# Kernel tuning notes

Measured on AMD Instinct MI355X. Metric: run time of the kernel, lower is better.

Reference implementation:

```python
import jax, jax.numpy as jnp
import numpy as np

NB_X = 32
NB_Y = 32
EPS = 1e-08


def setup_inputs() -> dict:
    key = jax.random.key(0)
    ks = jax.random.split(key, 10)
    B, L, F, H, D = 16, NB_X * NB_Y + 1, 768, 12, 64
    s = 0.02
    return {
        'x': jax.random.normal(ks[0], (B, L, F), dtype=jnp.float32),
        'wq': jax.random.normal(ks[1], (F, H, D), dtype=jnp.float32) * s,
        'bq': jnp.zeros((H, D), dtype=jnp.float32),
        'wk': jax.random.normal(ks[2], (F, H, D), dtype=jnp.float32) * s,
        'bk': jnp.zeros((H, D), dtype=jnp.float32),
        'wv': jax.random.normal(ks[3], (F, H, D), dtype=jnp.float32) * s,
        'bv': jnp.zeros((H, D), dtype=jnp.float32),
        'wo': jax.random.normal(ks[4], (H, D, F), dtype=jnp.float32) * s,
        'bo': jnp.zeros((F,), dtype=jnp.float32),
        'toeplitz_params': jax.random.normal(ks[5], (H, 4 * NB_X * NB_Y), dtype=jnp.float32),
    }


def _dist_index():
    # relative-position index over the 2D patch grid, flattened to (L0*L0,)
    gi = np.arange(NB_X)
    gj = np.arange(NB_Y)
    idx = ((gi[:, None, None, None] - gi[None, None, :, None] + NB_X) * 2 * NB_Y
           + gj[None, :, None, None] - gj[None, None, None, :] + NB_Y)
    return jnp.asarray(idx.reshape(-1), dtype=jnp.int32)


def reference(x, wq, bq, wk, bk, wv, bv, wo, bo, toeplitz_params):
    H, D = wq.shape[1], wq.shape[2]
    L0 = NB_X * NB_Y  # number of patch tokens (seq len = L0 + 1 with CLS)

    q = jnp.einsum('bqf,fhd->bqhd', x, wq) + bq
    k = jnp.einsum('bkf,fhd->bkhd', x, wk) + bk
    v = jnp.einsum('bkf,fhd->bkhd', x, wv) + bv

    # relu-kernelized scores
    q = jax.nn.relu(q / jnp.sqrt(jnp.float32(D))) + EPS
    k = jax.nn.relu(k) + EPS
    attn = jnp.einsum('bqhd,bkhd->bhqk', q, k)  # [B,H,L,L]

    # per-head Toeplitz relative-position mask via gather
    tm = jnp.take(toeplitz_params, _dist_index(), axis=1).reshape(H, L0, L0)
    tm = jnp.pad(tm, [[0, 0], [1, 0], [0, 0]], constant_values=1.0)
    tm = jnp.pad(tm, [[0, 0], [0, 0], [1, 0]], constant_values=1.0)

    attn = attn * jnp.abs(tm)[None] + EPS
    attn = attn / jnp.sum(attn, axis=-1, keepdims=True)  # sum-normalization

    out = jnp.einsum('bhqk,bkhd->bqhd', attn, v)
    return jnp.einsum('bqhd,hdf->bqf', out, wo) + bo
```

## Files before the change

kernel.cpp:

```cpp
#include <hip/hip_runtime.h>
#include <hip/hip_bf16.h>

#define BB 16
#define LQ 1025
#define FF 768
#define HH 12
#define DD 64
#define EPSF 1e-8f

typedef unsigned short u16;
typedef __attribute__((ext_vector_type(8))) short  bf16x8;
typedef __attribute__((ext_vector_type(4))) float  f32x4;

__device__ __forceinline__ float bf2f(u16 u) {
    union { unsigned int i; float f; } c;
    c.i = ((unsigned int)u) << 16;
    return c.f;
}

__device__ __forceinline__ u16 f2bf(float f) {
    union { float f; unsigned int i; } c;
    c.f = f;
    unsigned int x = c.i;
    unsigned int r = (x + 0x7fffu + ((x >> 16) & 1u)) >> 16;
    return (u16)r;
}

__global__ __launch_bounds__(256) void convert_x(
    const float* __restrict__ x, u16* __restrict__ xb, int n4)
{
    int i = blockIdx.x * blockDim.x + threadIdx.x;
    const int stride = gridDim.x * blockDim.x;
    for (; i < n4; i += stride) {
        float4 f = ((const float4*)x)[i];
        ushort4 o;
        o.x = f2bf(f.x); o.y = f2bf(f.y); o.z = f2bf(f.z); o.w = f2bf(f.w);
        ((ushort4*)xb)[i] = o;
    }
}

__global__ __launch_bounds__(256) void transpose_w(
    const float* __restrict__ wq, const float* __restrict__ wk,
    const float* __restrict__ wv, const float* __restrict__ wo,
    u16* __restrict__ wqt, u16* __restrict__ wkt,
    u16* __restrict__ wvt, u16* __restrict__ wot)
{
    const int z = blockIdx.z;
    const float* __restrict__ src = (z == 0) ? wq : (z == 1) ? wk : (z == 2) ? wv : wo;
    u16* __restrict__ dst         = (z == 0) ? wqt : (z == 1) ? wkt : (z == 2) ? wvt : wot;

    const int c0 = blockIdx.x * 64;
    const int r0 = blockIdx.y * 64;

    __shared__ u16 tile[64][72];

    const int t   = threadIdx.x;
    const int row = t >> 2;
    const int cs  = (t & 3) << 4;

    {
        const float* p = src + (size_t)(r0 + row) * 768 + c0 + cs;
#pragma unroll
        for (int q = 0; q < 4; ++q) {
            float4 f = *(const float4*)(p + 4 * q);
            ushort4 o;
            o.x = f2bf(f.x); o.y = f2bf(f.y); o.z = f2bf(f.z); o.w = f2bf(f.w);
            *(ushort4*)&tile[row][cs + 4 * q] = o;
        }
    }
    __syncthreads();
    {
        u16* p = dst + (size_t)(c0 + row) * 768 + r0 + cs;
#pragma unroll
        for (int q = 0; q < 4; ++q) {
            ushort4 o;
            o.x = tile[cs + 4 * q + 0][row];
            o.y = tile[cs + 4 * q + 1][row];
            o.z = tile[cs + 4 * q + 2][row];
            o.w = tile[cs + 4 * q + 3][row];
            *(ushort4*)(p + 4 * q) = o;
        }
    }
}

__global__ __launch_bounds__(256) void gemm_qkv_mfma(
    const u16* __restrict__ xb,
    const u16* __restrict__ wqt, const u16* __restrict__ wkt,
    const u16* __restrict__ wvt,
    const float* __restrict__ bq, const float* __restrict__ bk,
    const float* __restrict__ bv,
    u16* __restrict__ qbuf, u16* __restrict__ kbuf, u16* __restrict__ vbuf)
{
    const int M  = BB * LQ;
    const int m0 = blockIdx.x * 128;
    const int h  = blockIdx.y;
    const int n0 = h * 64;

    __shared__ u16 As[128][40];
    __shared__ u16 Bq[64][40];
    __shared__ u16 Bk[64][40];
    __shared__ u16 Bv[64][40];

    const int t    = threadIdx.x;
    const int wave = t >> 6;
    const int lane = t & 63;
    const int quad = lane >> 4;
    const int l16  = lane & 15;

    const int sm   = t >> 1;
    const int sseg = (t & 1) << 4;
    const int bn   = t >> 2;
    const int bseg = (t & 3) << 3;

    f32x4 acc[3][2][4];
#pragma unroll
    for (int ty = 0; ty < 3; ++ty)
#pragma unroll
        for (int i = 0; i < 2; ++i)
#pragma unroll
            for (int j = 0; j < 4; ++j)
                acc[ty][i][j] = (f32x4){0.f, 0.f, 0.f, 0.f};

    for (int k0 = 0; k0 < 768; k0 += 32) {
        __syncthreads();
        {
            int gm = m0 + sm;
            if (gm < M) {
                const uint4* p = (const uint4*)(xb + (size_t)gm * 768 + k0 + sseg);
                *(uint4*)&As[sm][sseg]     = p[0];
                *(uint4*)&As[sm][sseg + 8] = p[1];
            } else {
                uint4 z; z.x = 0; z.y = 0; z.z = 0; z.w = 0;
                *(uint4*)&As[sm][sseg]     = z;
                *(uint4*)&As[sm][sseg + 8] = z;
            }
        }
        {
            size_t off = (size_t)(n0 + bn) * 768 + k0 + bseg;
            *(uint4*)&Bq[bn][bseg] = *(const uint4*)(wqt + off);
            *(uint4*)&Bk[bn][bseg] = *(const uint4*)(wkt + off);
            *(uint4*)&Bv[bn][bseg] = *(const uint4*)(wvt + off);
        }
        __syncthreads();

        bf16x8 af0 = *(const bf16x8*)&As[(wave << 5) + l16][quad * 8];
        bf16x8 af1 = *(const bf16x8*)&As[(wave << 5) + 16 + l16][quad * 8];
#pragma unroll
        for (int j = 0; j < 4; ++j) {
            bf16x8 bq8 = *(const bf16x8*)&Bq[16 * j + l16][quad * 8];
            acc[0][0][j] = __builtin_amdgcn_mfma_f32_16x16x32_bf16(af0, bq8, acc[0][0][j], 0, 0, 0);
            acc[0][1][j] = __builtin_amdgcn_mfma_f32_16x16x32_bf16(af1, bq8, acc[0][1][j], 0, 0, 0);
            bf16x8 bk8 = *(const bf16x8*)&Bk[16 * j + l16][quad * 8];
            acc[1][0][j] = __builtin_amdgcn_mfma_f32_16x16x32_bf16(af0, bk8, acc[1][0][j], 0, 0, 0);
            acc[1][1][j] = __builtin_amdgcn_mfma_f32_16x16x32_bf16(af1, bk8, acc[1][1][j], 0, 0, 0);
            bf16x8 bv8 = *(const bf16x8*)&Bv[16 * j + l16][quad * 8];
            acc[2][0][j] = __builtin_amdgcn_mfma_f32_16x16x32_bf16(af0, bv8, acc[2][0][j], 0, 0, 0);
            acc[2][1][j] = __builtin_amdgcn_mfma_f32_16x16x32_bf16(af1, bv8, acc[2][1][j], 0, 0, 0);
        }
    }

#pragma unroll
    for (int i = 0; i < 2; ++i) {
#pragma unroll
        for (int reg = 0; reg < 4; ++reg) {
            int gm = m0 + (wave << 5) + (i << 4) + quad * 4 + reg;
            if (gm >= M) continue;
            int b_idx = gm / LQ;
            int l     = gm - b_idx * LQ;
            size_t obase = ((size_t)(b_idx * HH + h) * LQ + l) * 64;
#pragma unroll
            for (int j = 0; j < 4; ++j) {
                int d = 16 * j + l16;
                float fb = bq[n0 + d];
                float vq = acc[0][i][j][reg] + fb;
                vq = fmaxf(vq * 0.125f, 0.f) + EPSF;
                qbuf[obase + d] = f2bf(vq);
                float vk = acc[1][i][j][reg] + bk[n0 + d];
                vk = fmaxf(vk, 0.f) + EPSF;
                kbuf[obase + d] = f2bf(vk);
                float vv = acc[2][i][j][reg] + bv[n0 + d];
                vbuf[obase + d] = f2bf(vv);
            }
        }
    }
}

__global__ __launch_bounds__(256) void attn_fused(
    const u16* __restrict__ qbuf, const u16* __restrict__ kbuf,
    const u16* __restrict__ vbuf, const float* __restrict__ tp,
    u16* __restrict__ obuf)
{
    const int bh = blockIdx.y;
    const int b  = bh / HH;
    const int h  = bh - b * HH;
    const int q0 = blockIdx.x * 64;

    __shared__ u16 SQ[64][72];
    __shared__ u16 Ks[64][72];
    __shared__ u16 Vt[64][72];

    const int t    = threadIdx.x;
    const int wave = t >> 6;
    const int lane = t & 63;
    const int quad = lane >> 4;
    const int l16  = lane & 15;
    const int w16  = wave << 4;

    const size_t base  = (size_t)bh * LQ * 64;
    const int    hbase = h * 4096;

    {
        const int row = t >> 2;
        const int s0  = (t & 3) << 4;
        const int qi = q0 + row;
        if (qi < LQ) {
            const uint4* qp = (const uint4*)(qbuf + base + (size_t)qi * 64 + s0);
            *(uint4*)&SQ[row][s0]     = qp[0];
            *(uint4*)&SQ[row][s0 + 8] = qp[1];
        } else {
            uint4 z; z.x = 0; z.y = 0; z.z = 0; z.w = 0;
            *(uint4*)&SQ[row][s0]     = z;
            *(uint4*)&SQ[row][s0 + 8] = z;
        }
    }
    __syncthreads();

    bf16x8 qf0 = *(const bf16x8*)&SQ[w16 + l16][quad * 8];
    bf16x8 qf1 = *(const bf16x8*)&SQ[w16 + l16][32 + quad * 8];

    int  gqi_[4], gqj_[4];
    bool qv_[4], qc_[4];
#pragma unroll
    for (int reg = 0; reg < 4; ++reg) {
        int qi = q0 + w16 + quad * 4 + reg;
        qv_[reg] = (qi < LQ);
        qc_[reg] = (qi == 0);
        int qm1 = qi - 1;
        gqi_[reg] = (qv_[reg] && !qc_[reg]) ? (qm1 >> 5) : 0;
        gqj_[reg] = (qv_[reg] && !qc_[reg]) ? (qm1 & 31) : 0;
    }

    f32x4 acc_o[4];
#pragma unroll
    for (int dt = 0; dt < 4; ++dt) acc_o[dt] = (f32x4){0.f, 0.f, 0.f, 0.f};
    float den_acc[4] = {0.f, 0.f, 0.f, 0.f};

    for (int kt = 0; kt < 17; ++kt) {
        const int k0 = kt * 64;
        __syncthreads();

        {
            const int row = t >> 2;
            const int s0  = (t & 3) << 4;
            const int ki = k0 + row;
            if (ki < LQ) {
                const uint4* kp = (const uint4*)(kbuf + base + (size_t)ki * 64 + s0);
                *(uint4*)&Ks[row][s0]     = kp[0];
                *(uint4*)&Ks[row][s0 + 8] = kp[1];
                const ushort4* vp = (const ushort4*)(vbuf + base + (size_t)ki * 64 + s0);
                ushort4 v0 = vp[0], v1 = vp[1], v2 = vp[2], v3 = vp[3];
                Vt[s0 +  0][row] = v0.x; Vt[s0 +  1][row] = v0.y;
                Vt[s0 +  2][row] = v0.z; Vt[s0 +  3][row] = v0.w;
                Vt[s0 +  4][row] = v1.x; Vt[s0 +  5][row] = v1.y;
                Vt[s0 +  6][row] = v1.z; Vt[s0 +  7][row] = v1.w;
                Vt[s0 +  8][row] = v2.x; Vt[s0 +  9][row] = v2.y;
                Vt[s0 + 10][row] = v2.z; Vt[s0 + 11][row] = v2.w;
                Vt[s0 + 12][row] = v3.x; Vt[s0 + 13][row] = v3.y;
                Vt[s0 + 14][row] = v3.z; Vt[s0 + 15][row] = v3.w;
            } else {
                uint4 z; z.x = 0; z.y = 0; z.z = 0; z.w = 0;
                *(uint4*)&Ks[row][s0]     = z;
                *(uint4*)&Ks[row][s0 + 8] = z;
#pragma unroll
                for (int j = 0; j < 16; ++j) Vt[s0 + j][row] = 0;
            }
        }
        __syncthreads();

        f32x4 acc_s[4];
#pragma unroll
        for (int ct = 0; ct < 4; ++ct) {
            bf16x8 kf0 = *(const bf16x8*)&Ks[ct * 16 + l16][quad * 8];
            bf16x8 kf1 = *(const bf16x8*)&Ks[ct * 16 + l16][32 + quad * 8];
            f32x4 z = (f32x4){0.f, 0.f, 0.f, 0.f};
            z = __builtin_amdgcn_mfma_f32_16x16x32_bf16(qf0, kf0, z, 0, 0, 0);
            z = __builtin_amdgcn_mfma_f32_16x16x32_bf16(qf1, kf1, z, 0, 0, 0);
            acc_s[ct] = z;
        }

#pragma unroll
        for (int ct = 0; ct < 4; ++ct) {
            int ki = k0 + ct * 16 + l16;
            bool kvalid = (ki < LQ);
            bool kcls   = (ki == 0);
            int gki = 0, gkj = 0;
            if (kvalid && !kcls) { gki = (ki - 1) >> 5; gkj = (ki - 1) & 31; }
#pragma unroll
            for (int reg = 0; reg < 4; ++reg) {
                float sv = 0.f;
                if (qv_[reg] && kvalid) {
                    float tm = 1.f;
                    if (!qc_[reg] && !kcls) {
                        int idx = ((gqi_[reg] - gki + 32) << 6) + (gqj_[reg] - gkj + 32);
                        tm = fabsf(tp[hbase + idx]);
                    }
                    sv = acc_s[ct][reg] * tm + EPSF;
                }
                den_acc[reg] += sv;
                SQ[w16 + quad * 4 + reg][ct * 16 + l16] = f2bf(sv);
            }
        }
        __syncthreads();

        {
            bf16x8 a0 = *(const bf16x8*)&SQ[w16 + l16][quad * 8];
            bf16x8 a1 = *(const bf16x8*)&SQ[w16 + l16][32 + quad * 8];
#pragma unroll
            for (int dt = 0; dt < 4; ++dt) {
                bf16x8 b0 = *(const bf16x8*)&Vt[dt * 16 + l16][quad * 8];
                bf16x8 b1 = *(const bf16x8*)&Vt[dt * 16 + l16][32 + quad * 8];
                acc_o[dt] = __builtin_amdgcn_mfma_f32_16x16x32_bf16(a0, b0, acc_o[dt], 0, 0, 0);
                acc_o[dt] = __builtin_amdgcn_mfma_f32_16x16x32_bf16(a1, b1, acc_o[dt], 0, 0, 0);
            }
        }
    }

    float inv[4];
#pragma unroll
    for (int reg = 0; reg < 4; ++reg) {
        float r = den_acc[reg];
        r += __shfl_xor(r, 1);
        r += __shfl_xor(r, 2);
        r += __shfl_xor(r, 4);
        r += __shfl_xor(r, 8);
        inv[reg] = 1.f / r;
    }

#pragma unroll
    for (int reg = 0; reg < 4; ++reg) {
        int qi = q0 + w16 + quad * 4 + reg;
        if (qi >= LQ) continue;
        u16* p = obuf + ((size_t)(b * LQ + qi) * HH + h) * 64;
#pragma unroll
        for (int dt = 0; dt < 4; ++dt)
            p[dt * 16 + l16] = f2bf(acc_o[dt][reg] * inv[reg]);
    }
}

__global__ __launch_bounds__(256) void gemm_out_mfma(
    const u16* __restrict__ a, const u16* __restrict__ wot,
    const float* __restrict__ bo, float* __restrict__ out)
{
    const int M  = BB * LQ;
    const int m0 = blockIdx.x * 128;
    const int n0 = blockIdx.y * 64;

    __shared__ u16 As[128][40];
    __shared__ u16 Bs[64][40];

    const int t    = threadIdx.x;
    const int wave = t >> 6;
    const int lane = t & 63;
    const int quad = lane >> 4;
    const int l16  = lane & 15;

    const int sm   = t >> 1;
    const int sseg = (t & 1) << 4;
    const int bn   = t >> 2;
    const int bseg = (t & 3) << 3;

    f32x4 acc[2][4];
#pragma unroll
    for (int i = 0; i < 2; ++i)
#pragma unroll
        for (int j = 0; j < 4; ++j)
            acc[i][j] = (f32x4){0.f, 0.f, 0.f, 0.f};

    for (int k0 = 0; k0 < 768; k0 += 32) {
        __syncthreads();
        {
            int gm = m0 + sm;
            if (gm < M) {
                const uint4* p = (const uint4*)(a + (size_t)gm * 768 + k0 + sseg);
                *(uint4*)&As[sm][sseg]     = p[0];
                *(uint4*)&As[sm][sseg + 8] = p[1];
            } else {
                uint4 z; z.x = 0; z.y = 0; z.z = 0; z.w = 0;
                *(uint4*)&As[sm][sseg]     = z;
                *(uint4*)&As[sm][sseg + 8] = z;
            }
        }
        {
            *(uint4*)&Bs[bn][bseg] =
                *(const uint4*)(wot + (size_t)(n0 + bn) * 768 + k0 + bseg);
        }
        __syncthreads();

        bf16x8 af0 = *(const bf16x8*)&As[(wave << 5) + l16][quad * 8];
        bf16x8 af1 = *(const bf16x8*)&As[(wave << 5) + 16 + l16][quad * 8];
#pragma unroll
        for (int j = 0; j < 4; ++j) {
            bf16x8 b8 = *(const bf16x8*)&Bs[16 * j + l16][quad * 8];
            acc[0][j] = __builtin_amdgcn_mfma_f32_16x16x32_bf16(af0, b8, acc[0][j], 0, 0, 0);
            acc[1][j] = __builtin_amdgcn_mfma_f32_16x16x32_bf16(af1, b8, acc[1][j], 0, 0, 0);
        }
    }

#pragma unroll
    for (int i = 0; i < 2; ++i) {
#pragma unroll
        for (int reg = 0; reg < 4; ++reg) {
            int gm = m0 + (wave << 5) + (i << 4) + quad * 4 + reg;
            if (gm >= M) continue;
            float* p = out + (size_t)gm * 768;
#pragma unroll
            for (int j = 0; j < 4; ++j) {
                int n = n0 + 16 * j + l16;
                p[n] = acc[i][j][reg] + bo[n];
            }
        }
    }
}

extern "C" void kernel_launch(void* const* d_in, const int* in_sizes, int n_in,
                              void* d_out, int out_size, void* d_ws, size_t ws_size,
                              hipStream_t stream) {
    const float* x  = (const float*)d_in[0];
    const float* wq = (const float*)d_in[1];
    const float* bq = (const float*)d_in[2];
    const float* wk = (const float*)d_in[3];
    const float* bk = (const float*)d_in[4];
    const float* wv = (const float*)d_in[5];
    const float* bv = (const float*)d_in[6];
    const float* wo = (const float*)d_in[7];
    const float* bo = (const float*)d_in[8];
    const float* tp = (const float*)d_in[9];
    float* out = (float*)d_out;

    const size_t per = (size_t)BB * HH * LQ * DD;
    const size_t wsz = (size_t)FF * FF;
    u16* qbuf = (u16*)d_ws;
    u16* kbuf = qbuf + per;
    u16* vbuf = kbuf + per;
    u16* xobuf = vbuf + per;
    u16* wqt  = xobuf + per;
    u16* wkt  = wqt + wsz;
    u16* wvt  = wkt + wsz;
    u16* wot  = wvt + wsz;

    convert_x<<<2048, 256, 0, stream>>>(x, xobuf, (int)(per / 4));
    dim3 gt(12, 12, 4);
    transpose_w<<<gt, 256, 0, stream>>>(wq, wk, wv, wo, wqt, wkt, wvt, wot);

    dim3 g1(129, 12);
    gemm_qkv_mfma<<<g1, 256, 0, stream>>>(xobuf, wqt, wkt, wvt, bq, bk, bv,
                                          qbuf, kbuf, vbuf);

    dim3 g2(17, BB * HH);
    attn_fused<<<g2, 256, 0, stream>>>(qbuf, kbuf, vbuf, tp, xobuf);

    dim3 g3(129, 12);
    gemm_out_mfma<<<g3, 256, 0, stream>>>(xobuf, wot, bo, out);
}
```

Baseline: 547.1 us.

## Pre-transpose V, pad Toeplitz table, and register-prefetch K/V tiles in attention

Adds a kernel that stores V transposed into a padded global buffer, so the attention kernel can load V^T with vector stores instead of scattered shared-memory writes. A second new kernel builds a per-head padded abs(Toeplitz) table. The table folds the CLS and out-of-range cases into constant 0 or 1 entries, which lets the inner loop drop its branches and use precomputed indices that are decremented each tile. K/V tiles for the next iteration are prefetched into registers, and the score MFMA operands are swapped so each lane owns one query row, which simplifies the denominator reduction. The cost is two extra launches, extra global traffic for the V transpose, and buffer aliasing that reuses workspace regions.

```diff
diff --git a/kernel.cpp b/kernel.cpp
--- a/kernel.cpp
+++ b/kernel.cpp
@@ -7,6 +7,10 @@
 #define HH 12
 #define DD 64
 #define EPSF 1e-8f
+
+#define TPSTRIDE 6400
+#define QPART_CLS 6270
+#define VSTRIDE 1040
 
 typedef unsigned short u16;
 typedef __attribute__((ext_vector_type(8))) short  bf16x8;
@@ -79,6 +83,64 @@
             o.z = tile[cs + 4 * q + 2][row];
             o.w = tile[cs + 4 * q + 3][row];
             *(ushort4*)(p + 4 * q) = o;
+        }
+    }
+}
+
+__global__ __launch_bounds__(256) void build_tpa(
+    const float* __restrict__ tp, float* __restrict__ tpa)
+{
+    int i = blockIdx.x * 256 + threadIdx.x;
+    if (i >= HH * TPSTRIDE) return;
+    int h = i / TPSTRIDE, j = i - h * TPSTRIDE;
+    float v;
+    if (j < 64) v = 0.f;
+    else if (j < 64 + 4096) v = fabsf(tp[h * 4096 + (j - 64)]);
+    else v = 1.f;
+    tpa[i] = v;
+}
+
+__global__ __launch_bounds__(256) void transpose_v(
+    const u16* __restrict__ vbuf, u16* __restrict__ vtbuf)
+{
+    const int bh = blockIdx.y;
+    const int lt = blockIdx.x;
+    __shared__ u16 tile[64][65];
+    const int t   = threadIdx.x;
+    const int row = t >> 2;
+    const int seg = (t & 3) << 4;
+
+    {
+        int l = lt * 64 + row;
+        if (l < LQ) {
+            const ushort4* p = (const ushort4*)(vbuf + ((size_t)bh * LQ + l) * 64 + seg);
+#pragma unroll
+            for (int q = 0; q < 4; ++q) {
+                ushort4 a = p[q];
+                tile[row][seg + 4 * q + 0] = a.x;
+                tile[row][seg + 4 * q + 1] = a.y;
+                tile[row][seg + 4 * q + 2] = a.z;
+                tile[row][seg + 4 * q + 3] = a.w;
+            }
+        } else {
+#pragma unroll
+            for (int j = 0; j < 16; ++j) tile[row][seg + j] = 0;
+        }
+    }
+    __syncthreads();
+    {
+        int kbase = lt * 64 + seg;
+        if (kbase + 16 <= VSTRIDE) {
+            u16* q = vtbuf + (size_t)bh * 64 * VSTRIDE + (size_t)row * VSTRIDE + kbase;
+#pragma unroll
+            for (int g = 0; g < 4; ++g) {
+                ushort4 o;
+                o.x = tile[seg + 4 * g + 0][row];
+                o.y = tile[seg + 4 * g + 1][row];
+                o.z = tile[seg + 4 * g + 2][row];
+                o.w = tile[seg + 4 * g + 3][row];
+                *(ushort4*)(q + 4 * g) = o;
+            }
         }
     }
 }
@@ -171,8 +233,7 @@
 #pragma unroll
             for (int j = 0; j < 4; ++j) {
                 int d = 16 * j + l16;
-                float fb = bq[n0 + d];
-                float vq = acc[0][i][j][reg] + fb;
+                float vq = acc[0][i][j][reg] + bq[n0 + d];
                 vq = fmaxf(vq * 0.125f, 0.f) + EPSF;
                 qbuf[obase + d] = f2bf(vq);
                 float vk = acc[1][i][j][reg] + bk[n0 + d];
@@ -187,7 +248,7 @@
 
 __global__ __launch_bounds__(256) void attn_fused(
     const u16* __restrict__ qbuf, const u16* __restrict__ kbuf,
-    const u16* __restrict__ vbuf, const float* __restrict__ tp,
+    const u16* __restrict__ vtbuf, const float* __restrict__ tpa,
     u16* __restrict__ obuf)
 {
     const int bh = blockIdx.y;
@@ -207,74 +268,81 @@
     const int w16  = wave << 4;
 
     const size_t base  = (size_t)bh * LQ * 64;
-    const int    hbase = h * 4096;
+    const size_t vbase = (size_t)bh * 64 * VSTRIDE;
+    const float* tb = tpa + h * TPSTRIDE;
+
+    const int srow = t >> 2;
+    const int sseg = (t & 3) << 4;
 
     {
-        const int row = t >> 2;
-        const int s0  = (t & 3) << 4;
-        const int qi = q0 + row;
-        if (qi < LQ) {
-            const uint4* qp = (const uint4*)(qbuf + base + (size_t)qi * 64 + s0);
-            *(uint4*)&SQ[row][s0]     = qp[0];
-            *(uint4*)&SQ[row][s0 + 8] = qp[1];
-        } else {
-            uint4 z; z.x = 0; z.y = 0; z.z = 0; z.w = 0;
-            *(uint4*)&SQ[row][s0]     = z;
-            *(uint4*)&SQ[row][s0 + 8] = z;
-        }
-    }
+        const uint4* qp = (const uint4*)(qbuf + base + (size_t)(q0 + srow) * 64 + sseg);
+        *(uint4*)&SQ[srow][sseg]     = qp[0];
+        *(uint4*)&SQ[srow][sseg + 8] = qp[1];
+    }
+
+    const int qi = q0 + w16 + l16;
+    int qpart;
+    if (qi == 0) qpart = QPART_CLS;
+    else { int qm1 = qi - 1; qpart = (((qm1 >> 5) + 32) << 6) + (qm1 & 31) + 32; }
+
+    int idx[16];
+#pragma unroll
+    for (int ct = 0; ct < 4; ++ct)
+#pragma unroll
+        for (int reg = 0; reg < 4; ++reg) {
+            int km1 = ct * 16 + quad * 4 + reg - 1;
+            idx[ct * 4 + reg] = 64 + qpart - (((km1 >> 5) << 6) + (km1 & 31));
+        }
+
+    uint4 kr0, kr1, vr0, vr1;
+    {
+        uint4 z; z.x = 0; z.y = 0; z.z = 0; z.w = 0;
+        int ki = srow;
+        if (ki < LQ) {
+            const uint4* kp = (const uint4*)(kbuf + base + (size_t)ki * 64 + sseg);
+            kr0 = kp[0]; kr1 = kp[1];
+        } else { kr0 = z; kr1 = z; }
+        const uint4* vp = (const uint4*)(vtbuf + vbase + (size_t)srow * VSTRIDE + sseg);
+        vr0 = vp[0]; vr1 = vp[1];
+    }
+
     __syncthreads();
 
     bf16x8 qf0 = *(const bf16x8*)&SQ[w16 + l16][quad * 8];
     bf16x8 qf1 = *(const bf16x8*)&SQ[w16 + l16][32 + quad * 8];
 
-    int  gqi_[4], gqj_[4];
-    bool qv_[4], qc_[4];
-#pragma unroll
-    for (int reg = 0; reg < 4; ++reg) {
-        int qi = q0 + w16 + quad * 4 + reg;
-        qv_[reg] = (qi < LQ);
-        qc_[reg] = (qi == 0);
-        int qm1 = qi - 1;
-        gqi_[reg] = (qv_[reg] && !qc_[reg]) ? (qm1 >> 5) : 0;
-        gqj_[reg] = (qv_[reg] && !qc_[reg]) ? (qm1 & 31) : 0;
-    }
-
     f32x4 acc_o[4];
 #pragma unroll
     for (int dt = 0; dt < 4; ++dt) acc_o[dt] = (f32x4){0.f, 0.f, 0.f, 0.f};
-    float den_acc[4] = {0.f, 0.f, 0.f, 0.f};
+    float den = 0.f;
 
     for (int kt = 0; kt < 17; ++kt) {
-        const int k0 = kt * 64;
-        __syncthreads();
-
-        {
-            const int row = t >> 2;
-            const int s0  = (t & 3) << 4;
-            const int ki = k0 + row;
+        __syncthreads();
+
+        *(uint4*)&Ks[srow][sseg]     = kr0;
+        *(uint4*)&Ks[srow][sseg + 8] = kr1;
+        *(uint4*)&Vt[srow][sseg]     = vr0;
+        *(uint4*)&Vt[srow][sseg + 8] = vr1;
+
+        float tmv[16];
+#pragma unroll
+        for (int e = 0; e < 16; ++e) tmv[e] = tb[idx[e]];
+
+        if (kt < 16) {
+            uint4 z; z.x = 0; z.y = 0; z.z = 0; z.w = 0;
+            int k0n = (kt + 1) * 64;
+            int ki = k0n + srow;
             if (ki < LQ) {
-                const uint4* kp = (const uint4*)(kbuf + base + (size_t)ki * 64 + s0);
-                *(uint4*)&Ks[row][s0]     = kp[0];
-                *(uint4*)&Ks[row][s0 + 8] = kp[1];
-                const ushort4* vp = (const ushort4*)(vbuf + base + (size_t)ki * 64 + s0);
-                ushort4 v0 = vp[0], v1 = vp[1], v2 = vp[2], v3 = vp[3];
-                Vt[s0 +  0][row] = v0.x; Vt[s0 +  1][row] = v0.y;
-                Vt[s0 +  2][row] = v0.z; Vt[s0 +  3][row] = v0.w;
-                Vt[s0 +  4][row] = v1.x; Vt[s0 +  5][row] = v1.y;
-                Vt[s0 +  6][row] = v1.z; Vt[s0 +  7][row] = v1.w;
-                Vt[s0 +  8][row] = v2.x; Vt[s0 +  9][row] = v2.y;
-                Vt[s0 + 10][row] = v2.z; Vt[s0 + 11][row] = v2.w;
-                Vt[s0 + 12][row] = v3.x; Vt[s0 + 13][row] = v3.y;
-                Vt[s0 + 14][row] = v3.z; Vt[s0 + 15][row] = v3.w;
-            } else {
-                uint4 z; z.x = 0; z.y = 0; z.z = 0; z.w = 0;
-                *(uint4*)&Ks[row][s0]     = z;
-                *(uint4*)&Ks[row][s0 + 8] = z;
-#pragma unroll
-                for (int j = 0; j < 16; ++j) Vt[s0 + j][row] = 0;
-            }
-        }
+                const uint4* kp = (const uint4*)(kbuf + base + (size_t)ki * 64 + sseg);
+                kr0 = kp[0]; kr1 = kp[1];
+            } else { kr0 = z; kr1 = z; }
+            int vcol = k0n + sseg;
+            if (vcol + 16 <= VSTRIDE) {
+                const uint4* vp = (const uint4*)(vtbuf + vbase + (size_t)srow * VSTRIDE + vcol);
+                vr0 = vp[0]; vr1 = vp[1];
+            } else { vr0 = z; vr1 = z; }
+        }
+
         __syncthreads();
 
         f32x4 acc_s[4];
@@ -283,33 +351,27 @@
             bf16x8 kf0 = *(const bf16x8*)&Ks[ct * 16 + l16][quad * 8];
             bf16x8 kf1 = *(const bf16x8*)&Ks[ct * 16 + l16][32 + quad * 8];
             f32x4 z = (f32x4){0.f, 0.f, 0.f, 0.f};
-            z = __builtin_amdgcn_mfma_f32_16x16x32_bf16(qf0, kf0, z, 0, 0, 0);
-            z = __builtin_amdgcn_mfma_f32_16x16x32_bf16(qf1, kf1, z, 0, 0, 0);
+            z = __builtin_amdgcn_mfma_f32_16x16x32_bf16(kf0, qf0, z, 0, 0, 0);
+            z = __builtin_amdgcn_mfma_f32_16x16x32_bf16(kf1, qf1, z, 0, 0, 0);
             acc_s[ct] = z;
         }
 
+        if (kt == 0) { if (quad == 0) tmv[0] = 1.0f; }
+
 #pragma unroll
         for (int ct = 0; ct < 4; ++ct) {
-            int ki = k0 + ct * 16 + l16;
-            bool kvalid = (ki < LQ);
-            bool kcls   = (ki == 0);
-            int gki = 0, gkj = 0;
-            if (kvalid && !kcls) { gki = (ki - 1) >> 5; gkj = (ki - 1) & 31; }
-#pragma unroll
-            for (int reg = 0; reg < 4; ++reg) {
-                float sv = 0.f;
-                if (qv_[reg] && kvalid) {
-                    float tm = 1.f;
-                    if (!qc_[reg] && !kcls) {
-                        int idx = ((gqi_[reg] - gki + 32) << 6) + (gqj_[reg] - gkj + 32);
-                        tm = fabsf(tp[hbase + idx]);
-                    }
-                    sv = acc_s[ct][reg] * tm + EPSF;
-                }
-                den_acc[reg] += sv;
-                SQ[w16 + quad * 4 + reg][ct * 16 + l16] = f2bf(sv);
-            }
-        }
+            float s0 = acc_s[ct][0] * tmv[ct * 4 + 0] + EPSF;
+            float s1 = acc_s[ct][1] * tmv[ct * 4 + 1] + EPSF;
+            float s2 = acc_s[ct][2] * tmv[ct * 4 + 2] + EPSF;
+            float s3 = acc_s[ct][3] * tmv[ct * 4 + 3] + EPSF;
+            den += (s0 + s1) + (s2 + s3);
+            ushort4 w;
+            w.x = f2bf(s0); w.y = f2bf(s1); w.z = f2bf(s2); w.w = f2bf(s3);
+            *(ushort4*)&SQ[w16 + l16][ct * 16 + quad * 4] = w;
+        }
+#pragma unroll
+        for (int e = 0; e < 16; ++e) idx[e] -= 128;
+
         __syncthreads();
 
         {
@@ -325,25 +387,21 @@
         }
     }
 
-    float inv[4];
+    den += __shfl_xor(den, 16);
+    den += __shfl_xor(den, 32);
+    float invd = 1.f / den;
+
 #pragma unroll
     for (int reg = 0; reg < 4; ++reg) {
-        float r = den_acc[reg];
-        r += __shfl_xor(r, 1);
-        r += __shfl_xor(r, 2);
-        r += __shfl_xor(r, 4);
-        r += __shfl_xor(r, 8);
-        inv[reg] = 1.f / r;
-    }
-
-#pragma unroll
-    for (int reg = 0; reg < 4; ++reg) {
-        int qi = q0 + w16 + quad * 4 + reg;
-        if (qi >= LQ) continue;
-        u16* p = obuf + ((size_t)(b * LQ + qi) * HH + h) * 64;
-#pragma unroll
-        for (int dt = 0; dt < 4; ++dt)
-            p[dt * 16 + l16] = f2bf(acc_o[dt][reg] * inv[reg]);
+        int r = quad * 4 + reg;
+        float iv = __shfl(invd, r, 64);
+        int qrow = q0 + w16 + r;
+        if (qrow < LQ) {
+            u16* p = obuf + ((size_t)(b * LQ + qrow) * HH + h) * 64;
+#pragma unroll
+            for (int dt = 0; dt < 4; ++dt)
+                p[dt * 16 + l16] = f2bf(acc_o[dt][reg] * iv);
+        }
     }
 }
 
@@ -439,26 +497,35 @@
 
     const size_t per = (size_t)BB * HH * LQ * DD;
     const size_t wsz = (size_t)FF * FF;
-    u16* qbuf = (u16*)d_ws;
-    u16* kbuf = qbuf + per;
-    u16* vbuf = kbuf + per;
-    u16* xobuf = vbuf + per;
-    u16* wqt  = xobuf + per;
-    u16* wkt  = wqt + wsz;
-    u16* wvt  = wkt + wsz;
-    u16* wot  = wvt + wsz;
-
-    convert_x<<<2048, 256, 0, stream>>>(x, xobuf, (int)(per / 4));
+    u16* ws16  = (u16*)d_ws;
+    u16* qbuf  = ws16;
+    u16* kbuf  = qbuf + per;
+    u16* vbuf  = kbuf + per;
+    u16* xb    = vbuf + per;
+    u16* wqt   = xb + per;
+    u16* wkt   = wqt + wsz;
+    u16* wvt   = wkt + wsz;
+    u16* wot   = wvt + wsz;
+    float* tpa = (float*)(wot + wsz);
+
+    u16* vtbuf = xb;
+    u16* obuf  = vbuf;
+
+    convert_x<<<2048, 256, 0, stream>>>(x, xb, (int)(per / 4));
     dim3 gt(12, 12, 4);
     transpose_w<<<gt, 256, 0, stream>>>(wq, wk, wv, wo, wqt, wkt, wvt, wot);
+    build_tpa<<<(HH * TPSTRIDE + 255) / 256, 256, 0, stream>>>(tp, tpa);
 
     dim3 g1(129, 12);
-    gemm_qkv_mfma<<<g1, 256, 0, stream>>>(xobuf, wqt, wkt, wvt, bq, bk, bv,
+    gemm_qkv_mfma<<<g1, 256, 0, stream>>>(xb, wqt, wkt, wvt, bq, bk, bv,
                                           qbuf, kbuf, vbuf);
 
+    dim3 gv(17, BB * HH);
+    transpose_v<<<gv, 256, 0, stream>>>(vbuf, vtbuf);
+
     dim3 g2(17, BB * HH);
-    attn_fused<<<g2, 256, 0, stream>>>(qbuf, kbuf, vbuf, tp, xobuf);
+    attn_fused<<<g2, 256, 0, stream>>>(qbuf, kbuf, vtbuf, tpa, obuf);
 
     dim3 g3(129, 12);
-    gemm_out_mfma<<<g3, 256, 0, stream>>>(xobuf, wot, bo, out);
-}
+    gemm_out_mfma<<<g3, 256, 0, stream>>>(obuf, wot, bo, out);
+}
```

Result: faster. 484.8 us (-11.4%).
